# Kernel tuning notes

Hardware: AMD Instinct MI355X
Metric: run time of the kernel (lower is better)

The kernel has to match this reference:

```python
import jax, jax.numpy as jnp
import numpy as np

N = 50000   # nodes
E = 1600000 # edges
F = 128     # node feature dim
D_ENC, D_EMB, D_H = 32, 12, 128
TEMPERATURE = 10.0


def _dense(key, fan_in, fan_out):
    kw, kb = jax.random.split(key)
    W = jax.random.normal(kw, (fan_in, fan_out), jnp.float32) * (1.0 / jnp.sqrt(fan_in))
    b = jnp.zeros((fan_out,), jnp.float32)
    return W, b


def setup_inputs() -> dict:
    key = jax.random.key(0)
    ks = jax.random.split(key, 12)
    nodes = jax.random.normal(ks[0], (N, F), jnp.float32)
    senders = jax.random.randint(ks[1], (E,), 0, N, dtype=jnp.int32)
    receivers = jax.random.randint(ks[2], (E,), 0, N, dtype=jnp.int32)
    W_enc, b_enc = _dense(ks[3], F, D_ENC)
    W_inf, b_inf = _dense(ks[4], D_ENC + 1, 1)
    W_emb, b_emb = _dense(ks[5], F, D_EMB)
    W1, b1 = _dense(ks[6], D_EMB, D_H)
    W2, b2 = _dense(ks[7], D_H, D_H)
    Wy, by = _dense(ks[8], D_H, 1)
    Wx, bx = _dense(ks[9], D_H, 4)
    return {"nodes": nodes, "senders": senders, "receivers": receivers,
            "W_enc": W_enc, "b_enc": b_enc, "W_inf": W_inf, "b_inf": b_inf,
            "W_emb": W_emb, "b_emb": b_emb, "W1": W1, "b1": b1,
            "W2": W2, "b2": b2, "Wy": Wy, "by": by, "Wx": Wx, "bx": bx}


def reference(nodes, senders, receivers, W_enc, b_enc, W_inf, b_inf,
              W_emb, b_emb, W1, b1, W2, b2, Wy, by, Wx, bx):
    n_nodes = nodes.shape[0]
    # EncodeNet: Dense(32) + relu
    vodes = jax.nn.relu(nodes @ W_enc + b_enc)                      # [N, 32]
    # compute_pure_message: gather by senders, scatter-add by receivers
    msg = jax.ops.segment_sum(vodes[senders], receivers, num_segments=n_nodes)
    vodes = vodes + msg                                             # [N, 32]
    # concat last raw node feature
    vodes = jnp.concatenate([vodes, nodes[:, -1:]], axis=1)         # [N, 33]
    # InfluenceNet: Dense(1), softmax over nodes
    influence = vodes @ W_inf + b_inf                               # [N, 1]
    attention = jax.nn.softmax(influence, axis=0)                   # [N, 1]
    # EmbedNet: Dense(12); softmax-weighted pooling over nodes
    emb = nodes @ W_emb + b_emb                                     # [N, 12]
    g = jnp.sum(emb * attention, axis=0)                            # [12]
    # ActNet head
    h = jax.nn.relu(g @ W1 + b1)
    h = jax.nn.relu(h @ W2 + b2)
    value = h @ Wy + by                                             # [1]
    logits = h @ Wx + bx                                            # [4]
    return (logits / TEMPERATURE, value)
```

## Files before the change

### kernel.cpp

```cpp
#include <hip/hip_runtime.h>
#include <hip/hip_bf16.h>


#define NF 128
#define DENC 32
#define DEMB 12
#define DH 128

#define NSLICE 128
#define NRANGE 2
#define R_SCAT 25000

template <int NJ, int LDW>
__device__ __forceinline__ void gemv_rows(
    const float4* __restrict__ x4p, const float* __restrict__ W,
    int jbase, const float* __restrict__ bias, float* acc, float& x_last)
{
#pragma unroll
    for (int j = 0; j < NJ; j++) acc[j] = bias[jbase + j];
#pragma unroll 2
    for (int c = 0; c < 8; c++) {
        float4 xa = x4p[4 * c + 0];
        float4 xb = x4p[4 * c + 1];
        float4 xc = x4p[4 * c + 2];
        float4 xd = x4p[4 * c + 3];
        float xs[16] = {xa.x, xa.y, xa.z, xa.w, xb.x, xb.y, xb.z, xb.w,
                        xc.x, xc.y, xc.z, xc.w, xd.x, xd.y, xd.z, xd.w};
#pragma unroll
        for (int u = 0; u < 16; u++) {
            const int k = 16 * c + u;
#pragma unroll
            for (int j = 0; j < NJ; j++)
                acc[j] = fmaf(xs[u], W[k * LDW + jbase + j], acc[j]);
        }
        if (c == 7) x_last = xd.w;
    }
}

__global__ __launch_bounds__(256) void k1_node(
    const float* __restrict__ nodes,
    const float* __restrict__ W_enc, const float* __restrict__ b_enc,
    const float* __restrict__ W_inf, const float* __restrict__ b_inf,
    const float* __restrict__ W_emb, const float* __restrict__ b_emb,
    float* __restrict__ p, float* __restrict__ inflb, float* __restrict__ embT,
    unsigned* __restrict__ cnt, int n_nodes)
{
    __shared__ float tabp[3][64];
    const int tid  = threadIdx.x;
    const int lane = tid & 63;
    const int wv   = __builtin_amdgcn_readfirstlane(tid >> 6);
    const int node = blockIdx.x * 64 + lane;
    const bool ok  = (node < n_nodes);

    if (blockIdx.x == 0 && tid == 0) *cnt = 0u;

    const float4* x4p = ok ? (const float4*)(nodes + (size_t)node * NF)
                           : (const float4*)nodes;

    float x127 = 0.f;
    if (wv == 3) {
        float acc[DEMB];
        gemv_rows<DEMB, DEMB>(x4p, W_emb, 0, b_emb, acc, x127);
        if (ok) {
#pragma unroll
            for (int j = 0; j < DEMB; j++)
                embT[(size_t)j * n_nodes + node] = acc[j];
        }
    } else {
        const int jbase = __builtin_amdgcn_readfirstlane(wv * 11);
        float pp = 0.f;
        if (wv == 2) {
            float acc[10];
            gemv_rows<10, DENC>(x4p, W_enc, jbase, b_enc, acc, x127);
#pragma unroll
            for (int j = 0; j < 10; j++)
                pp += fmaxf(acc[j], 0.f) * W_inf[jbase + j];
        } else {
            float acc[11];
            gemv_rows<11, DENC>(x4p, W_enc, jbase, b_enc, acc, x127);
#pragma unroll
            for (int j = 0; j < 11; j++)
                pp += fmaxf(acc[j], 0.f) * W_inf[jbase + j];
        }
        tabp[wv][lane] = pp;
    }
    __syncthreads();

    if (wv == 0 && ok) {
        float pn = tabp[0][lane] + tabp[1][lane] + tabp[2][lane];
        p[node] = pn;
        inflb[node] = pn + x127 * W_inf[DENC] + b_inf[0];
    }
}

__global__ __launch_bounds__(1024) void k2_scatter(
    const int* __restrict__ senders, const int* __restrict__ recvs,
    const float* __restrict__ p, float* __restrict__ rep,
    int n_nodes, int n_edges)
{
    extern __shared__ float tab[];
    const int slice = blockIdx.x >> 1;
    const int rng_i = blockIdx.x & 1;
    const int e0 = (int)((long long)n_edges * slice / NSLICE);
    const int e1 = (int)((long long)n_edges * (slice + 1) / NSLICE);
    const int lo = rng_i * R_SCAT;
    const int rng = min(R_SCAT, n_nodes - lo);

    float4* tab4 = (float4*)tab;
    for (int i = threadIdx.x; i < (rng + 3) / 4; i += 1024)
        tab4[i] = make_float4(0.f, 0.f, 0.f, 0.f);
    __syncthreads();

    const int ae0 = (e0 + 3) & ~3;
    const int ae1 = e1 & ~3;
    for (int e = e0 + (int)threadIdx.x; e < ae0; e += 1024) {
        unsigned rr = (unsigned)(recvs[e] - lo);
        if (rr < (unsigned)rng) atomicAdd(&tab[rr], p[senders[e]]);
    }
    const int4* r4 = (const int4*)recvs;
    const int4* s4 = (const int4*)senders;
    for (int i = ae0 / 4 + (int)threadIdx.x; i < ae1 / 4; i += 1024) {
        int4 r = r4[i];
        int4 s = s4[i];
        unsigned rr;
        rr = (unsigned)(r.x - lo); if (rr < (unsigned)rng) atomicAdd(&tab[rr], p[s.x]);
        rr = (unsigned)(r.y - lo); if (rr < (unsigned)rng) atomicAdd(&tab[rr], p[s.y]);
        rr = (unsigned)(r.z - lo); if (rr < (unsigned)rng) atomicAdd(&tab[rr], p[s.z]);
        rr = (unsigned)(r.w - lo); if (rr < (unsigned)rng) atomicAdd(&tab[rr], p[s.w]);
    }
    for (int e = ae1 + (int)threadIdx.x; e < e1; e += 1024) {
        unsigned rr = (unsigned)(recvs[e] - lo);
        if (rr < (unsigned)rng) atomicAdd(&tab[rr], p[senders[e]]);
    }
    __syncthreads();

    float* __restrict__ dst = rep + (size_t)slice * n_nodes + lo;
    for (int i = threadIdx.x; i < rng / 4; i += 1024)
        ((float4*)dst)[i] = tab4[i];
    for (int i = (rng & ~3) + threadIdx.x; i < rng; i += 1024)
        dst[i] = tab[i];
}

__global__ __launch_bounds__(256) void k34_soft(
    const float* __restrict__ inflb, const float* __restrict__ rep,
    const float* __restrict__ embT, float* __restrict__ psum,
    unsigned* __restrict__ cnt,
    const float* __restrict__ W1, const float* __restrict__ b1,
    const float* __restrict__ W2, const float* __restrict__ b2,
    const float* __restrict__ Wy, const float* __restrict__ by,
    const float* __restrict__ Wx, const float* __restrict__ bx,
    float* __restrict__ out, int n_nodes, int nblk)
{
    __shared__ float tab[4][64];
    const int tid  = threadIdx.x;
    const int lane = tid & 63;
    const int wv   = __builtin_amdgcn_readfirstlane(tid >> 6);
    const int node = blockIdx.x * 64 + lane;
    const bool ok  = (node < n_nodes);

    float s = 0.f;
    if (ok) {
        const float* r = rep + (size_t)(32 * wv) * n_nodes + node;
#pragma unroll 8
        for (int i = 0; i < NSLICE / 4; i++)
            s += r[(size_t)i * n_nodes];
    }
    tab[wv][lane] = s;
    __syncthreads();

    if (wv == 0) {
        float infl = ok ? inflb[node] + tab[0][lane] + tab[1][lane]
                          + tab[2][lane] + tab[3][lane]
                        : -1e30f;
        float m = infl;
#pragma unroll
        for (int off = 32; off; off >>= 1)
            m = fmaxf(m, __shfl_down(m, off, 64));
        m = __shfl(m, 0, 64);

        const float w = ok ? expf(infl - m) : 0.f;
        float v13[13];
        v13[0] = w;
#pragma unroll
        for (int j = 0; j < DEMB; j++)
            v13[1 + j] = ok ? w * embT[(size_t)j * n_nodes + node] : 0.f;

#pragma unroll
        for (int v = 0; v < 13; v++) {
            float x = v13[v];
#pragma unroll
            for (int off = 32; off; off >>= 1)
                x += __shfl_down(x, off, 64);
            v13[v] = x;
        }
        if (lane == 0) {
            psum[blockIdx.x * 14] = m;
#pragma unroll
            for (int v = 0; v < 13; v++)
                psum[blockIdx.x * 14 + 1 + v] = v13[v];
        }
    }
    __syncthreads();

    __shared__ int is_last;
    if (tid == 0) {
        __threadfence();
        unsigned old = atomicAdd(cnt, 1u);
        is_last = (old == (unsigned)(nblk - 1)) ? 1 : 0;
    }
    __syncthreads();
    if (!is_last) return;
    __threadfence();

    const int w4 = tid >> 6, l4 = tid & 63;

    float m = -1e30f;
    for (int b = tid; b < nblk; b += 256) m = fmaxf(m, psum[b * 14]);
#pragma unroll
    for (int off = 32; off; off >>= 1)
        m = fmaxf(m, __shfl_down(m, off, 64));
    __shared__ float smx[4];
    __shared__ float sM;
    if (l4 == 0) smx[w4] = m;
    __syncthreads();
    if (tid == 0)
        sM = fmaxf(fmaxf(smx[0], smx[1]), fmaxf(smx[2], smx[3]));
    __syncthreads();
    const float M = sM;

    float acc[13];
#pragma unroll
    for (int v = 0; v < 13; v++) acc[v] = 0.f;
    for (int b = tid; b < nblk; b += 256) {
        float sc = expf(psum[b * 14] - M);
#pragma unroll
        for (int v = 0; v < 13; v++)
            acc[v] = fmaf(sc, psum[b * 14 + 1 + v], acc[v]);
    }

    __shared__ float red[4][13];
#pragma unroll
    for (int v = 0; v < 13; v++) {
        float xx = acc[v];
#pragma unroll
        for (int off = 32; off; off >>= 1)
            xx += __shfl_down(xx, off, 64);
        if (l4 == 0) red[w4][v] = xx;
    }
    __syncthreads();

    __shared__ float g[DEMB];
    __shared__ float h1[DH];
    __shared__ float h2[DH];
    if (tid < DEMB) {
        float S = red[0][0] + red[1][0] + red[2][0] + red[3][0];
        g[tid] = (red[0][1 + tid] + red[1][1 + tid] +
                  red[2][1 + tid] + red[3][1 + tid]) / S;
    }
    __syncthreads();

    if (tid < DH) {
        float s1 = b1[tid];
#pragma unroll
        for (int i = 0; i < DEMB; i++) s1 = fmaf(g[i], W1[i * DH + tid], s1);
        h1[tid] = fmaxf(s1, 0.f);
    }
    __syncthreads();

    if (tid < DH) {
        float s2v = b2[tid];
        for (int i = 0; i < DH; i++) s2v = fmaf(h1[i], W2[i * DH + tid], s2v);
        h2[tid] = fmaxf(s2v, 0.f);
    }
    __syncthreads();

    if (tid < 4) {
        float lg = bx[tid];
        for (int i = 0; i < DH; i++) lg = fmaf(h2[i], Wx[i * 4 + tid], lg);
        out[tid] = lg / 10.0f;
    } else if (tid == 4) {
        float v = by[0];
        for (int i = 0; i < DH; i++) v = fmaf(h2[i], Wy[i], v);
        out[4] = v;
    }
}

extern "C" void kernel_launch(void* const* d_in, const int* in_sizes, int n_in,
                              void* d_out, int out_size, void* d_ws, size_t ws_size,
                              hipStream_t stream) {
    const float* nodes   = (const float*)d_in[0];
    const int*   senders = (const int*)d_in[1];
    const int*   recvs   = (const int*)d_in[2];
    const float* W_enc   = (const float*)d_in[3];
    const float* b_enc   = (const float*)d_in[4];
    const float* W_inf   = (const float*)d_in[5];
    const float* b_inf   = (const float*)d_in[6];
    const float* W_emb   = (const float*)d_in[7];
    const float* b_emb   = (const float*)d_in[8];
    const float* W1      = (const float*)d_in[9];
    const float* b1      = (const float*)d_in[10];
    const float* W2      = (const float*)d_in[11];
    const float* b2      = (const float*)d_in[12];
    const float* Wy      = (const float*)d_in[13];
    const float* by      = (const float*)d_in[14];
    const float* Wx      = (const float*)d_in[15];
    const float* bx      = (const float*)d_in[16];
    float* out = (float*)d_out;

    const int n_nodes = in_sizes[0] / NF;
    const int n_edges = in_sizes[1];
    const int nb64 = (n_nodes + 63) / 64;

    float* ws    = (float*)d_ws;
    float* p     = ws;
    float* inflb = ws + n_nodes;
    float* embT  = ws + 2 * (size_t)n_nodes;
    float* rep   = ws + 14 * (size_t)n_nodes;
    float* psum  = ws + (14 + NSLICE) * (size_t)n_nodes;
    unsigned* cnt = (unsigned*)(psum + (size_t)nb64 * 14 + 4);

    (void)hipFuncSetAttribute((const void*)k2_scatter,
                              hipFuncAttributeMaxDynamicSharedMemorySize,
                              R_SCAT * (int)sizeof(float));

    hipLaunchKernelGGL(k1_node, dim3(nb64), dim3(256), 0, stream,
                       nodes, W_enc, b_enc, W_inf, b_inf, W_emb, b_emb,
                       p, inflb, embT, cnt, n_nodes);
    hipLaunchKernelGGL(k2_scatter, dim3(NSLICE * NRANGE), dim3(1024),
                       R_SCAT * sizeof(float), stream,
                       senders, recvs, p, rep, n_nodes, n_edges);
    hipLaunchKernelGGL(k34_soft, dim3(nb64), dim3(256), 0, stream,
                       inflb, rep, embT, psum, cnt,
                       W1, b1, W2, b2, Wy, by, Wx, bx, out, n_nodes, nb64);
}
```

Baseline: 174.1 us.

## Tile scatter partials by node chunk and split scatter into four node ranges

The scatter kernel now splits nodes into four 16000-entry ranges, using a static shared table and 512-thread blocks instead of two 25000-entry dynamic tables with 1024 threads. Per-slice partial sums are stored in a chunk-major layout (64-node chunk × slice × 64). This lets the reduction kernel read one contiguous block per node group instead of strided rows spaced n_nodes apart. The trade-off is that each edge slice is now read four times instead of twice, in return for smaller shared tables that may allow more blocks resident per CU and better locality in the final reduction.

```diff
diff --git a/kernel.cpp b/kernel.cpp
--- a/kernel.cpp
+++ b/kernel.cpp
@@ -8,8 +8,9 @@
 #define DH 128
 
 #define NSLICE 128
-#define NRANGE 2
-#define R_SCAT 25000
+#define NRANGE 4
+#define R_SCAT 16000
+#define ROWB (NSLICE*64)
 
 template <int NJ, int LDW>
 __device__ __forceinline__ void gemv_rows(
@@ -93,33 +94,33 @@
     }
 }
 
-__global__ __launch_bounds__(1024) void k2_scatter(
+__global__ __launch_bounds__(512) void k2_scatter(
     const int* __restrict__ senders, const int* __restrict__ recvs,
-    const float* __restrict__ p, float* __restrict__ rep,
+    const float* __restrict__ p, float* __restrict__ rep2,
     int n_nodes, int n_edges)
 {
-    extern __shared__ float tab[];
-    const int slice = blockIdx.x >> 1;
-    const int rng_i = blockIdx.x & 1;
+    __shared__ float tab[R_SCAT];
+    const int slice = blockIdx.x >> 2;
+    const int rng_i = blockIdx.x & 3;
     const int e0 = (int)((long long)n_edges * slice / NSLICE);
     const int e1 = (int)((long long)n_edges * (slice + 1) / NSLICE);
     const int lo = rng_i * R_SCAT;
     const int rng = min(R_SCAT, n_nodes - lo);
 
     float4* tab4 = (float4*)tab;
-    for (int i = threadIdx.x; i < (rng + 3) / 4; i += 1024)
+    for (int i = threadIdx.x; i < (rng + 3) / 4; i += 512)
         tab4[i] = make_float4(0.f, 0.f, 0.f, 0.f);
     __syncthreads();
 
     const int ae0 = (e0 + 3) & ~3;
     const int ae1 = e1 & ~3;
-    for (int e = e0 + (int)threadIdx.x; e < ae0; e += 1024) {
+    for (int e = e0 + (int)threadIdx.x; e < ae0; e += 512) {
         unsigned rr = (unsigned)(recvs[e] - lo);
         if (rr < (unsigned)rng) atomicAdd(&tab[rr], p[senders[e]]);
     }
     const int4* r4 = (const int4*)recvs;
     const int4* s4 = (const int4*)senders;
-    for (int i = ae0 / 4 + (int)threadIdx.x; i < ae1 / 4; i += 1024) {
+    for (int i = ae0 / 4 + (int)threadIdx.x; i < ae1 / 4; i += 512) {
         int4 r = r4[i];
         int4 s = s4[i];
         unsigned rr;
@@ -128,21 +129,25 @@
         rr = (unsigned)(r.z - lo); if (rr < (unsigned)rng) atomicAdd(&tab[rr], p[s.z]);
         rr = (unsigned)(r.w - lo); if (rr < (unsigned)rng) atomicAdd(&tab[rr], p[s.w]);
     }
-    for (int e = ae1 + (int)threadIdx.x; e < e1; e += 1024) {
+    for (int e = ae1 + (int)threadIdx.x; e < e1; e += 512) {
         unsigned rr = (unsigned)(recvs[e] - lo);
         if (rr < (unsigned)rng) atomicAdd(&tab[rr], p[senders[e]]);
     }
     __syncthreads();
 
-    float* __restrict__ dst = rep + (size_t)slice * n_nodes + lo;
-    for (int i = threadIdx.x; i < rng / 4; i += 1024)
-        ((float4*)dst)[i] = tab4[i];
-    for (int i = (rng & ~3) + threadIdx.x; i < rng; i += 1024)
-        dst[i] = tab[i];
+    float4* dst4 = (float4*)(rep2 + (size_t)(lo >> 6) * ROWB + slice * 64);
+    for (int i4 = threadIdx.x; i4 < rng / 4; i4 += 512) {
+        const int chunk = i4 >> 4;
+        const int col4  = i4 & 15;
+        dst4[(size_t)chunk * (ROWB / 4) + col4] = tab4[i4];
+    }
+    for (int i = (rng & ~3) + threadIdx.x; i < rng; i += 512)
+        rep2[(size_t)(lo >> 6) * ROWB + (size_t)(i >> 6) * ROWB
+             + slice * 64 + (i & 63)] = tab[i];
 }
 
 __global__ __launch_bounds__(256) void k34_soft(
-    const float* __restrict__ inflb, const float* __restrict__ rep,
+    const float* __restrict__ inflb, const float* __restrict__ rep2,
     const float* __restrict__ embT, float* __restrict__ psum,
     unsigned* __restrict__ cnt,
     const float* __restrict__ W1, const float* __restrict__ b1,
@@ -158,14 +163,14 @@
     const int node = blockIdx.x * 64 + lane;
     const bool ok  = (node < n_nodes);
 
-    float s = 0.f;
-    if (ok) {
-        const float* r = rep + (size_t)(32 * wv) * n_nodes + node;
+    {
+        const float* base = rep2 + (size_t)blockIdx.x * ROWB + 32 * wv * 64 + lane;
+        float s = 0.f;
 #pragma unroll 8
-        for (int i = 0; i < NSLICE / 4; i++)
-            s += r[(size_t)i * n_nodes];
-    }
-    tab[wv][lane] = s;
+        for (int i = 0; i < 32; i++)
+            s += base[i * 64];
+        tab[wv][lane] = ok ? s : 0.f;
+    }
     __syncthreads();
 
     if (wv == 0) {
@@ -315,21 +320,16 @@
     float* p     = ws;
     float* inflb = ws + n_nodes;
     float* embT  = ws + 2 * (size_t)n_nodes;
-    float* rep   = ws + 14 * (size_t)n_nodes;
-    float* psum  = ws + (14 + NSLICE) * (size_t)n_nodes;
+    float* rep2  = ws + 14 * (size_t)n_nodes;
+    float* psum  = rep2 + (size_t)nb64 * ROWB;
     unsigned* cnt = (unsigned*)(psum + (size_t)nb64 * 14 + 4);
-
-    (void)hipFuncSetAttribute((const void*)k2_scatter,
-                              hipFuncAttributeMaxDynamicSharedMemorySize,
-                              R_SCAT * (int)sizeof(float));
 
     hipLaunchKernelGGL(k1_node, dim3(nb64), dim3(256), 0, stream,
                        nodes, W_enc, b_enc, W_inf, b_inf, W_emb, b_emb,
                        p, inflb, embT, cnt, n_nodes);
-    hipLaunchKernelGGL(k2_scatter, dim3(NSLICE * NRANGE), dim3(1024),
-                       R_SCAT * sizeof(float), stream,
-                       senders, recvs, p, rep, n_nodes, n_edges);
+    hipLaunchKernelGGL(k2_scatter, dim3(NSLICE * NRANGE), dim3(512), 0, stream,
+                       senders, recvs, p, rep2, n_nodes, n_edges);
     hipLaunchKernelGGL(k34_soft, dim3(nb64), dim3(256), 0, stream,
-                       inflb, rep, embT, psum, cnt,
+                       inflb, rep2, embT, psum, cnt,
                        W1, b1, W2, b2, Wy, by, Wx, bx, out, n_nodes, nb64);
 }
```

Result: no change. 175.6 us (+0.8%).
